# Performance work log

Hardware: AMD Instinct MI355X
Metric: run time of the kernel (lower is better)

The kernel has to match this reference:

```python
import jax, jax.numpy as jnp
from jax import lax
import numpy as np

IMG = 1024          # original image H = W
HD = WD = 256       # detection feature map (stride 4)
CD = 128            # detection feature channels
HS = WS = 512       # segmentation feature map (stride 2)
CS = 32             # segmentation feature channels
FC = 1024           # detection head conv / fc filters
K = 2000            # pre-NMS topk
MAX_OUT = 500       # max proposals after NMS
NMS_THR = 1.0       # distance threshold in detection-grid units
CROP = 48           # instance crop size (instance_crop_size // 2)
CI = 64             # instance conv channels


def _conv(x, w, b):
    # x: [H,W,Cin] single map -> same-padded conv
    y = lax.conv_general_dilated(x[None], w, (1, 1), 'SAME',
                                 dimension_numbers=('NHWC', 'HWIO', 'NHWC'))[0]
    return y + b


def _conv_b(x, w, b):
    # x: [N,H,W,Cin] batched conv
    y = lax.conv_general_dilated(x, w, (1, 1), 'SAME',
                                 dimension_numbers=('NHWC', 'HWIO', 'NHWC'))
    return y + b


def setup_inputs() -> dict:
    key = jax.random.key(0)
    ks = jax.random.split(key, 10)
    s = 0.02
    return {
        'detection_features': jax.random.normal(ks[0], (HD, WD, CD), jnp.float32),
        'segmentation_features': jax.random.normal(ks[1], (HS, WS, CS), jnp.float32),
        'Wc': jax.random.normal(ks[2], (3, 3, CD, FC), jnp.float32) * s,
        'bc': jnp.zeros((FC,), jnp.float32),
        'Wfc': jax.random.normal(ks[3], (1, 1, FC, FC), jnp.float32) * s,
        'bfc': jnp.zeros((FC,), jnp.float32),
        'Ws': jax.random.normal(ks[4], (1, 1, FC, 1), jnp.float32) * s,
        'bs': jnp.zeros((1,), jnp.float32),
        'Wr': jax.random.normal(ks[5], (1, 1, FC, 2), jnp.float32) * s,
        'br': jnp.zeros((2,), jnp.float32),
        'Wi': jax.random.normal(ks[6], (3, 3, CS, CI), jnp.float32) * s,
        'bi': jnp.zeros((CI,), jnp.float32),
        'Wo': jax.random.normal(ks[7], (3, 3, CI, 1), jnp.float32) * s,
        'bo': jnp.zeros((1,), jnp.float32),
    }


def _forward(detection_features, segmentation_features,
             Wc, bc, Wfc, bfc, Ws, bs, Wr, br, Wi, bi, Wo, bo):
    x = jax.nn.relu(_conv(detection_features, Wc, bc))
    x = jax.nn.relu(_conv(x, Wfc, bfc))
    scores = jax.nn.sigmoid(_conv(x, Ws, bs))[..., 0]          # [HD,WD]
    reg = _conv(x, Wr, br)                                      # [HD,WD,2] offsets in grid units

    # ---- proposal_locations: decode, topk, distance-threshold NMS ----
    yy, xx = jnp.meshgrid(jnp.arange(HD, dtype=jnp.float32),
                          jnp.arange(WD, dtype=jnp.float32), indexing='ij')
    ctr = jnp.stack([yy, xx], axis=-1) + 0.5                    # cell centers
    locs = (ctr + reg) / jnp.array([HD, WD], jnp.float32)       # normalized [0,1]
    flat_scores = scores.reshape(-1)                            # [HD*WD]
    flat_locs = locs.reshape(-1, 2)

    top_s, top_i = lax.top_k(flat_scores, K)                    # pre-NMS topk (sorted desc)
    cand = flat_locs[top_i]                                     # [K,2] normalized

    grid_xy = cand * jnp.array([HD, WD], jnp.float32)           # grid-unit coords
    d2 = jnp.sum((grid_xy[:, None, :] - grid_xy[None, :, :]) ** 2, axis=-1)  # [K,K]
    close = d2 < (NMS_THR * NMS_THR)
    later = jnp.arange(K)[None, :] > jnp.arange(K)[:, None]

    def nms_body(i, suppressed):
        keep_i = jnp.logical_not(suppressed[i])
        return suppressed | (keep_i & close[i] & later[i])

    suppressed = lax.fori_loop(0, K, nms_body, jnp.zeros((K,), jnp.bool_))
    masked = jnp.where(suppressed, -1.0, top_s)
    proposed_scores, sel = lax.top_k(masked, MAX_OUT)           # [500]
    sel_norm = cand[sel]                                        # [500,2]
    decoded = sel_norm * jnp.float32(IMG)                       # pixel coords

    # ---- instance head: crop stride-2 seg features around each proposal ----
    seg_loc = decoded / 2.0
    start = jnp.clip(jnp.round(seg_loc - CROP / 2), 0, HS - CROP).astype(jnp.int32)  # [500,2]

    def crop_one(st):
        return lax.dynamic_slice(segmentation_features, (st[0], st[1], 0), (CROP, CROP, CS))

    crops = jax.vmap(crop_one)(start)                           # [500,48,48,CS]
    h = jax.nn.relu(_conv_b(crops, Wi, bi))                     # [500,48,48,CI]
    instance_output = jax.nn.sigmoid(_conv_b(h, Wo, bo))        # [500,48,48,1]

    cy, cx = jnp.meshgrid(jnp.arange(CROP), jnp.arange(CROP), indexing='ij')
    instance_coords = start[:, None, None, :] + jnp.stack([cy, cx], axis=-1)[None]  # [500,48,48,2]

    return proposed_scores, decoded, instance_output, instance_coords


def reference(detection_features, segmentation_features,
              Wc, bc, Wfc, bfc, Ws, bs, Wr, br, Wi, bi, Wo, bo):
    return _forward(detection_features, segmentation_features,
                    Wc, bc, Wfc, bfc, Ws, bs, Wr, br, Wi, bi, Wo, bo)
```

## Files before the change

### kernel.cpp

```cpp
#include <hip/hip_runtime.h>
#include <math.h>

#define KTOP 2000
#define MAXOUT 500
#define CANDCAP 4096
#define NSEL 3600
#define RCC 32
#define RC2 16

typedef __attribute__((ext_vector_type(8))) short short8;
typedef __attribute__((ext_vector_type(4))) float f32x4;
typedef __attribute__((ext_vector_type(4))) double f64x4;

__device__ __forceinline__ unsigned short f2bf(float f) {
  unsigned int u = __float_as_uint(f);
  unsigned int r = ((u >> 16) & 1u) + 0x7FFFu;
  return (unsigned short)((u + r) >> 16);
}

__device__ __forceinline__ void ld_lds16(const void* g, void* l) {
  __builtin_amdgcn_global_load_lds((const unsigned int*)g, (unsigned int*)l,
                                   16, 0, 0);
}

__device__ __forceinline__ void hard_barrier() {
  asm volatile("" ::: "memory");
  __builtin_amdgcn_sched_barrier(0);
  __builtin_amdgcn_s_barrier();
  __builtin_amdgcn_sched_barrier(0);
  asm volatile("" ::: "memory");
}

__global__ __launch_bounds__(256) void transpose_bf16_kernel(
    const float* __restrict__ W, unsigned short* __restrict__ WT, int K, int N)
{
  __shared__ float t[32][33];
  const int k0 = blockIdx.x << 5, n0 = blockIdx.y << 5;
  const int tid = threadIdx.x;
  const int r = tid >> 5, c = tid & 31;
#pragma unroll
  for (int p = 0; p < 4; ++p)
    t[r + (p << 3)][c] = W[(size_t)(k0 + r + (p << 3)) * N + n0 + c];
  __syncthreads();
#pragma unroll
  for (int p = 0; p < 4; ++p)
    WT[(size_t)(n0 + r + (p << 3)) * K + k0 + c] = f2bf(t[c][r + (p << 3)]);
}

__global__ __launch_bounds__(256) void prep_wib_kernel(
    const float* __restrict__ Wi, unsigned short* __restrict__ WiB)
{
  const int t = blockIdx.x * 256 + threadIdx.x;
  if (t < 9 * 64 * 32) {
    const int tap = t / 2048, r = t & 2047, co = r >> 5, ci = r & 31;
    WiB[t] = f2bf(Wi[((size_t)tap * 32 + ci) * 64 + co]);
  }
}

__global__ __launch_bounds__(256) void pad_df_bf16(
    const float* __restrict__ df, unsigned short* __restrict__ dfb)
{
  const int t = blockIdx.x * 256 + threadIdx.x;
  if (t >= 258 * 258 * 16) return;
  const int p = t >> 4;
  const int c8 = (t & 15) << 3;
  const int gy = p / 258 - 1, gx = p % 258 - 1;
  uint4 out = make_uint4(0, 0, 0, 0);
  if (gy >= 0 && gy < 256 && gx >= 0 && gx < 256) {
    const float* src = &df[((size_t)(gy * 256 + gx)) * 128 + c8];
    const float4 v0 = *(const float4*)src;
    const float4 v1 = *(const float4*)(src + 4);
    out.x = (unsigned int)f2bf(v0.x) | ((unsigned int)f2bf(v0.y) << 16);
    out.y = (unsigned int)f2bf(v0.z) | ((unsigned int)f2bf(v0.w) << 16);
    out.z = (unsigned int)f2bf(v1.x) | ((unsigned int)f2bf(v1.y) << 16);
    out.w = (unsigned int)f2bf(v1.z) | ((unsigned int)f2bf(v1.w) << 16);
  }
  *(uint4*)&dfb[(size_t)p * 128 + c8] = out;
}

__device__ __forceinline__ void ktile_phases(
    const unsigned short* __restrict__ A0, const unsigned short* __restrict__ B0,
    const int arow, const int brow, const int ok0, const int ok1,
    f32x4 (&acc)[8][4])
{
  short8 Af[4][2], Bf[2][2][2];
#pragma unroll
  for (int m = 0; m < 4; ++m) {
    Af[m][0] = *(const short8*)&A0[((arow + (m << 4)) << 6) + ok0];
    Af[m][1] = *(const short8*)&A0[((arow + (m << 4)) << 6) + ok1];
  }
#pragma unroll
  for (int n = 0; n < 2; ++n) {
    Bf[0][n][0] = *(const short8*)&B0[((brow + (n << 4)) << 6) + ok0];
    Bf[0][n][1] = *(const short8*)&B0[((brow + (n << 4)) << 6) + ok1];
  }
  hard_barrier();
  __builtin_amdgcn_s_setprio(1);
#pragma unroll
  for (int m = 0; m < 4; ++m)
#pragma unroll
    for (int n = 0; n < 2; ++n) {
      acc[m][n] = __builtin_amdgcn_mfma_f32_16x16x32_bf16(Af[m][0], Bf[0][n][0], acc[m][n], 0, 0, 0);
      acc[m][n] = __builtin_amdgcn_mfma_f32_16x16x32_bf16(Af[m][1], Bf[0][n][1], acc[m][n], 0, 0, 0);
    }
  __builtin_amdgcn_s_setprio(0);
  hard_barrier();
#pragma unroll
  for (int n = 0; n < 2; ++n) {
    Bf[1][n][0] = *(const short8*)&B0[((brow + ((n + 2) << 4)) << 6) + ok0];
    Bf[1][n][1] = *(const short8*)&B0[((brow + ((n + 2) << 4)) << 6) + ok1];
  }
  hard_barrier();
  __builtin_amdgcn_s_setprio(1);
#pragma unroll
  for (int m = 0; m < 4; ++m)
#pragma unroll
    for (int n = 0; n < 2; ++n) {
      acc[m][n + 2] = __builtin_amdgcn_mfma_f32_16x16x32_bf16(Af[m][0], Bf[1][n][0], acc[m][n + 2], 0, 0, 0);
      acc[m][n + 2] = __builtin_amdgcn_mfma_f32_16x16x32_bf16(Af[m][1], Bf[1][n][1], acc[m][n + 2], 0, 0, 0);
    }
  __builtin_amdgcn_s_setprio(0);
  hard_barrier();
#pragma unroll
  for (int m = 0; m < 4; ++m) {
    Af[m][0] = *(const short8*)&A0[((arow + 64 + (m << 4)) << 6) + ok0];
    Af[m][1] = *(const short8*)&A0[((arow + 64 + (m << 4)) << 6) + ok1];
  }
  hard_barrier();
  __builtin_amdgcn_s_setprio(1);
#pragma unroll
  for (int m = 0; m < 4; ++m)
#pragma unroll
    for (int n = 0; n < 2; ++n) {
      acc[m + 4][n + 2] = __builtin_amdgcn_mfma_f32_16x16x32_bf16(Af[m][0], Bf[1][n][0], acc[m + 4][n + 2], 0, 0, 0);
      acc[m + 4][n + 2] = __builtin_amdgcn_mfma_f32_16x16x32_bf16(Af[m][1], Bf[1][n][1], acc[m + 4][n + 2], 0, 0, 0);
    }
  __builtin_amdgcn_s_setprio(0);
  hard_barrier();
  __builtin_amdgcn_s_setprio(1);
#pragma unroll
  for (int m = 0; m < 4; ++m)
#pragma unroll
    for (int n = 0; n < 2; ++n) {
      acc[m + 4][n] = __builtin_amdgcn_mfma_f32_16x16x32_bf16(Af[m][0], Bf[0][n][0], acc[m + 4][n], 0, 0, 0);
      acc[m + 4][n] = __builtin_amdgcn_mfma_f32_16x16x32_bf16(Af[m][1], Bf[0][n][1], acc[m + 4][n], 0, 0, 0);
    }
  __builtin_amdgcn_s_setprio(0);
  hard_barrier();
}

__global__ __launch_bounds__(512) void conv1_mfma(
    const unsigned short* __restrict__ dfb, const unsigned short* __restrict__ WcT,
    const float* __restrict__ bc, unsigned short* __restrict__ x1b, int pt0)
{
  __shared__ __align__(16) unsigned short smem[65536];
  const int tid = threadIdx.x;
  const int wv = tid >> 6, lane = tid & 63;
  const int wr = wv >> 2, wc = wv & 3;
  const int l15 = lane & 15, quad = lane >> 4;
  const int n0 = blockIdx.x << 8;
  const int lm0 = blockIdx.y << 8;
  const int Pbase = (pt0 << 6) + lm0;
  const int y = Pbase >> 8;
  const int tr = tid >> 3, g8 = tid & 7;
  const int xg = ((g8 ^ (tr & 7)) << 4);
  const int axr = l15 & 7;
  const int ok0 = ((quad ^ axr) << 3);
  const int ok1 = (((4 + quad) ^ axr) << 3);
  const int arow = (wr << 7) + l15;
  const int brow = (wc << 6) + l15;

  float bcv[4];
#pragma unroll
  for (int j = 0; j < 4; ++j) bcv[j] = bc[n0 + (wc << 6) + (j << 4) + l15];

  f32x4 acc[8][4];
  const f32x4 z4 = {0.f, 0.f, 0.f, 0.f};
#pragma unroll
  for (int i = 0; i < 8; ++i)
#pragma unroll
    for (int j = 0; j < 4; ++j) acc[i][j] = z4;

  const char* WB = (const char*)WcT + ((size_t)(n0 + tr) * 1152) * 2 + xg;
  unsigned short* lA = &smem[(tr << 6) + (g8 << 3)];

  auto issue = [&](int kt, int buf) {
    const int tap = kt >> 1, ci0 = (kt & 1) << 6;
    const int dy = tap / 3 - 1, dx = tap % 3 - 1;
    const char* Ab = (const char*)dfb +
        (((size_t)((y + dy + 1) * 258 + dx + 1)) * 128 + ci0) * 2 +
        (size_t)tr * 256 + xg;
    unsigned short* la = lA + buf * 32768;
    unsigned short* lb = la + 16384;
    const char* Bb = WB + (size_t)kt * 128;
#pragma unroll
    for (int i = 0; i < 4; ++i)
      ld_lds16(Ab + (size_t)i * 16384, la + i * 4096);
#pragma unroll
    for (int i = 0; i < 4; ++i)
      ld_lds16(Bb + (size_t)i * 147456, lb + i * 4096);
  };

  issue(0, 0);
  issue(1, 1);
#pragma unroll 2
  for (int kt = 0; kt < 18; ++kt) {
    const int buf = kt & 1;
    if (kt < 17) asm volatile("s_waitcnt vmcnt(8)" ::: "memory");
    else         asm volatile("s_waitcnt vmcnt(0)" ::: "memory");
    hard_barrier();
    ktile_phases(&smem[buf * 32768], &smem[buf * 32768 + 16384],
                 arow, brow, ok0, ok1, acc);
    if (kt < 16) issue(kt + 2, buf);
  }

#pragma unroll
  for (int m = 0; m < 8; ++m)
#pragma unroll
    for (int n = 0; n < 4; ++n) {
      const int col = n0 + (wc << 6) + (n << 4) + l15;
      const float bb = bcv[n];
#pragma unroll
      for (int rg = 0; rg < 4; ++rg) {
        const int row = lm0 + (wr << 7) + (m << 4) + (quad << 2) + rg;
        const float v = fmaxf(acc[m][n][rg] + bb, 0.f);
        x1b[(size_t)row * 1024 + col] = f2bf(v);
      }
    }
}

__global__ __launch_bounds__(512) void fc_mfma(
    const unsigned short* __restrict__ x1b, const unsigned short* __restrict__ WfcT,
    const float* __restrict__ bfc, const float* __restrict__ Wsc,
    float* __restrict__ part, int pt0)
{
  __shared__ __align__(16) unsigned short smem[65536];
  const int tid = threadIdx.x;
  const int wv = tid >> 6, lane = tid & 63;
  const int wr = wv >> 2, wc = wv & 3;
  const int l15 = lane & 15, quad = lane >> 4;
  const int n0 = blockIdx.x << 8;
  const int lm0 = blockIdx.y << 8;
  const int Pbase = (pt0 << 6) + lm0;
  const int tr = tid >> 3, g8 = tid & 7;
  const int xg = ((g8 ^ (tr & 7)) << 4);
  const int axr = l15 & 7;
  const int ok0 = ((quad ^ axr) << 3);
  const int ok1 = (((4 + quad) ^ axr) << 3);
  const int arow = (wr << 7) + l15;
  const int brow = (wc << 6) + l15;

  float wsv[4], bfv[4];
#pragma unroll
  for (int j = 0; j < 4; ++j) {
    const int col = n0 + (wc << 6) + (j << 4) + l15;
    wsv[j] = Wsc[col];
    bfv[j] = bfc[col];
  }

  f32x4 acc[8][4];
  const f32x4 z4 = {0.f, 0.f, 0.f, 0.f};
#pragma unroll
  for (int i = 0; i < 8; ++i)
#pragma unroll
    for (int j = 0; j < 4; ++j) acc[i][j] = z4;

  const char* AB = (const char*)x1b + ((size_t)(lm0 + tr) * 1024) * 2 + xg;
  const char* WB = (const char*)WfcT + ((size_t)(n0 + tr) * 1024) * 2 + xg;
  unsigned short* lA = &smem[(tr << 6) + (g8 << 3)];

  auto issue = [&](int kt, int buf) {
    unsigned short* la = lA + buf * 32768;
    unsigned short* lb = la + 16384;
    const char* Ab = AB + (size_t)kt * 128;
    const char* Bb = WB + (size_t)kt * 128;
#pragma unroll
    for (int i = 0; i < 4; ++i)
      ld_lds16(Ab + (size_t)i * 131072, la + i * 4096);
#pragma unroll
    for (int i = 0; i < 4; ++i)
      ld_lds16(Bb + (size_t)i * 131072, lb + i * 4096);
  };

  issue(0, 0);
  issue(1, 1);
#pragma unroll 2
  for (int kt = 0; kt < 16; ++kt) {
    const int buf = kt & 1;
    if (kt < 15) asm volatile("s_waitcnt vmcnt(8)" ::: "memory");
    else         asm volatile("s_waitcnt vmcnt(0)" ::: "memory");
    hard_barrier();
    ktile_phases(&smem[buf * 32768], &smem[buf * 32768 + 16384],
                 arow, brow, ok0, ok1, acc);
    if (kt < 14) issue(kt + 2, buf);
  }

  float* red = (float*)smem;
#pragma unroll
  for (int m = 0; m < 8; ++m)
#pragma unroll
    for (int rg = 0; rg < 4; ++rg) {
      float ps = 0.f;
#pragma unroll
      for (int n = 0; n < 4; ++n) {
        const float v = fmaxf(acc[m][n][rg] + bfv[n], 0.f);
        ps = fmaf(v, wsv[n], ps);
      }
#pragma unroll
      for (int off = 1; off <= 8; off <<= 1)
        ps += __shfl_xor(ps, off, 64);
      if (l15 == 0) {
        const int row = (wr << 7) + (m << 4) + (quad << 2) + rg;
        red[row * 5 + wc] = ps;
      }
    }
  __syncthreads();
  if (tid < 256) {
    float s = 0.f;
#pragma unroll
    for (int w8 = 0; w8 < 4; ++w8) s += red[tid * 5 + w8];
    part[(size_t)blockIdx.x * 65536 + Pbase + tid] = s;
  }
}

__global__ __launch_bounds__(256) void head_finalize_kernel(
    const float* __restrict__ part, const float* __restrict__ bs,
    float* __restrict__ scores)
{
  const int pix = blockIdx.x * 256 + threadIdx.x;
  float s = 0.f;
#pragma unroll
  for (int cb = 0; cb < 4; ++cb) s += part[(size_t)cb * 65536 + pix];
  s += bs[0];
  scores[pix] = 1.f / (1.f + expf(-s));
}

__global__ __launch_bounds__(1024) void select_kernel(
    const float* __restrict__ scores, unsigned int* __restrict__ cand_idx,
    unsigned int* __restrict__ cand_cnt)
{
  __shared__ unsigned int hist[256];
  __shared__ unsigned int sh_prefix, sh_sub;
  __shared__ int scan_s[1024];
  const int tid = threadIdx.x;

  unsigned int prefix = 0u;
  int need = NSEL;
  for (int byte = 3; byte >= 0; --byte) {
    if (tid < 256) hist[tid] = 0u;
    __syncthreads();
    const int sh = byte * 8;
    const unsigned int mhi = (byte == 3) ? 0u : (0xFFFFFFFFu << (sh + 8));
    for (int i = tid; i < 65536; i += 1024) {
      const unsigned int b = __float_as_uint(scores[i]);
      if ((b & mhi) == prefix) atomicAdd(&hist[(b >> sh) & 255u], 1u);
    }
    __syncthreads();
    for (int off = 1; off < 256; off <<= 1) {
      unsigned int add = 0u;
      if (tid < 256 && tid + off < 256) add = hist[tid + off];
      __syncthreads();
      if (tid < 256) hist[tid] += add;
      __syncthreads();
    }
    if (tid < 256) {
      const unsigned int sv = hist[tid];
      const unsigned int above = (tid == 255) ? 0u : hist[tid + 1];
      if ((int)above < need && (int)sv >= need) {
        sh_prefix = prefix | ((unsigned)tid << sh);
        sh_sub = above;
      }
    }
    __syncthreads();
    prefix = sh_prefix;
    need -= (int)sh_sub;
    __syncthreads();
  }
  const float thr = __uint_as_float(prefix);

  const int b0 = tid << 6;
  int my = 0;
  for (int k = 0; k < 64; ++k)
    if (scores[b0 + k] >= thr) ++my;
  scan_s[tid] = my;
  __syncthreads();
  for (int off = 1; off < 1024; off <<= 1) {
    const int a = scan_s[tid];
    const int b = (tid >= off) ? scan_s[tid - off] : 0;
    __syncthreads();
    scan_s[tid] = a + b;
    __syncthreads();
  }
  int pos = scan_s[tid] - my;
  const int total = scan_s[1023];
  for (int k = 0; k < 64; ++k) {
    if (scores[b0 + k] >= thr) {
      if (pos < CANDCAP) cand_idx[pos] = (unsigned int)(b0 + k);
      ++pos;
    }
  }
  if (tid == 0)
    *cand_cnt = (unsigned int)(total > CANDCAP ? CANDCAP : total);
}

#define PSTR 133
__global__ __launch_bounds__(512) void rescore_conv(
    const float* __restrict__ df, const float* __restrict__ Wc,
    const float* __restrict__ bc,
    const unsigned int* __restrict__ cand_idx,
    const unsigned int* __restrict__ cand_cnt,
    double* __restrict__ x1g)
{
  __shared__ double patt[RCC * PSTR];
  __shared__ int rrs[RCC], ccs[RCC];
  const int cnt = (int)*cand_cnt;
  const int nb = blockIdx.x & 1;
  const int c0 = (blockIdx.x >> 1) * RCC;
  if (c0 >= cnt) return;
  const int tid = threadIdx.x;
  const int wv = tid >> 6, lane = tid & 63;
  const int m = lane & 15, quad = lane >> 4;
  const int co_base = (nb << 9) + (wv << 6);

  if (tid < RCC) {
    const int slot = (c0 + tid < cnt) ? c0 + tid : c0;
    const unsigned int idx = cand_idx[slot];
    rrs[tid] = (int)(idx >> 8); ccs[tid] = (int)(idx & 255u);
  }

  f64x4 acc[2][4];
  const f64x4 z4 = {0.0, 0.0, 0.0, 0.0};
#pragma unroll
  for (int ct = 0; ct < 2; ++ct)
#pragma unroll
    for (int t = 0; t < 4; ++t) acc[ct][t] = z4;

  for (int tap = 0; tap < 9; ++tap) {
    const int dy = tap / 3 - 1, dx = tap % 3 - 1;
    __syncthreads();
    for (int p = tid; p < RCC * 128; p += 512) {
      const int c = p >> 7, ci = p & 127;
      const int gy = rrs[c] + dy, gx = ccs[c] + dx;
      float v = 0.f;
      if (gy >= 0 && gy < 256 && gx >= 0 && gx < 256)
        v = df[((size_t)((gy << 8) + gx)) * 128 + ci];
      patt[c * PSTR + ci] = (double)v;
    }
    __syncthreads();
    const float* wrow = &Wc[(size_t)(tap * 128 + quad) * 1024 + co_base + m];
    float wf[4];
#pragma unroll
    for (int t = 0; t < 4; ++t) wf[t] = wrow[t << 4];
    for (int k4 = 0; k4 < 32; ++k4) {
      float wn[4];
      if (k4 + 1 < 32) {
#pragma unroll
        for (int t = 0; t < 4; ++t)
          wn[t] = wrow[(size_t)((k4 + 1) << 2) * 1024 + (t << 4)];
      }
      const double a0 = patt[m * PSTR + (k4 << 2) + quad];
      const double a1 = patt[(16 + m) * PSTR + (k4 << 2) + quad];
#pragma unroll
      for (int t = 0; t < 4; ++t)
        acc[0][t] = __builtin_amdgcn_mfma_f64_16x16x4f64(a0, (double)wf[t], acc[0][t], 0, 0, 0);
#pragma unroll
      for (int t = 0; t < 4; ++t)
        acc[1][t] = __builtin_amdgcn_mfma_f64_16x16x4f64(a1, (double)wf[t], acc[1][t], 0, 0, 0);
      if (k4 + 1 < 32) {
#pragma unroll
        for (int t = 0; t < 4; ++t) wf[t] = wn[t];
      }
    }
  }
#pragma unroll
  for (int ct = 0; ct < 2; ++ct)
#pragma unroll
    for (int t = 0; t < 4; ++t) {
      const int co = co_base + (t << 4) + m;
      const double bb = (double)bc[co];
#pragma unroll
      for (int rg = 0; rg < 4; ++rg) {
        const int cand = (ct << 4) + (quad << 2) + rg;
        if (c0 + cand < cnt) {
          const double v = acc[ct][t][rg] + bb;
          x1g[(size_t)(c0 + cand) * 1024 + co] = v > 0.0 ? v : 0.0;
        }
      }
    }
}

__global__ __launch_bounds__(512) void rescore_fc(
    const double* __restrict__ x1g, const float* __restrict__ Wfc,
    const float* __restrict__ bfc, const float* __restrict__ Wsc,
    const float* __restrict__ bs, const float* __restrict__ Wrg,
    const float* __restrict__ br,
    const unsigned int* __restrict__ cand_cnt,
    unsigned long long* __restrict__ cand_sb,
    double* __restrict__ cand_ry, double* __restrict__ cand_rx)
{
  __shared__ double xbuf[16 * PSTR];
  __shared__ double partw[3][8][16];
  const int cnt = (int)*cand_cnt;
  const int c0 = blockIdx.x * RC2;
  if (c0 >= cnt) return;
  const int tid = threadIdx.x;
  const int wv = tid >> 6, lane = tid & 63;
  const int m = lane & 15, quad = lane >> 4;
  const int co_base = wv << 7;

  f64x4 acc[8];
  const f64x4 z4 = {0.0, 0.0, 0.0, 0.0};
#pragma unroll
  for (int t = 0; t < 8; ++t) acc[t] = z4;

  for (int kc = 0; kc < 8; ++kc) {
    __syncthreads();
    for (int p = tid; p < 2048; p += 512) {
      const int c = p >> 7, k = p & 127;
      const int row = (c0 + c < cnt) ? c0 + c : c0;
      xbuf[c * PSTR + k] = x1g[(size_t)row * 1024 + (kc << 7) + k];
    }
    __syncthreads();
    const float* wrow = &Wfc[(size_t)((kc << 7) + quad) * 1024 + co_base + m];
    float wf[8];
#pragma unroll
    for (int t = 0; t < 8; ++t) wf[t] = wrow[t << 4];
    for (int k4 = 0; k4 < 32; ++k4) {
      float wn[8];
      if (k4 + 1 < 32) {
#pragma unroll
        for (int t = 0; t < 8; ++t)
          wn[t] = wrow[(size_t)((k4 + 1) << 2) * 1024 + (t << 4)];
      }
      const double a = xbuf[m * PSTR + (k4 << 2) + quad];
#pragma unroll
      for (int t = 0; t < 8; ++t)
        acc[t] = __builtin_amdgcn_mfma_f64_16x16x4f64(a, (double)wf[t], acc[t], 0, 0, 0);
      if (k4 + 1 < 32) {
#pragma unroll
        for (int t = 0; t < 8; ++t) wf[t] = wn[t];
      }
    }
  }

  double ps[4] = {0, 0, 0, 0}, py[4] = {0, 0, 0, 0}, px[4] = {0, 0, 0, 0};
#pragma unroll
  for (int t = 0; t < 8; ++t) {
    const int co = co_base + (t << 4) + m;
    const double bfv = (double)bfc[co];
    const double wsv = (double)Wsc[co];
    const double w0 = (double)Wrg[co * 2], w1 = (double)Wrg[co * 2 + 1];
#pragma unroll
    for (int rg = 0; rg < 4; ++rg) {
      double v = acc[t][rg] + bfv;
      v = v > 0.0 ? v : 0.0;
      ps[rg] = fma(v, wsv, ps[rg]);
      py[rg] = fma(v, w0, py[rg]);
      px[rg] = fma(v, w1, px[rg]);
    }
  }
#pragma unroll
  for (int off = 1; off <= 8; off <<= 1) {
#pragma unroll
    for (int rg = 0; rg < 4; ++rg) {
      ps[rg] += __shfl_xor(ps[rg], off, 64);
      py[rg] += __shfl_xor(py[rg], off, 64);
      px[rg] += __shfl_xor(px[rg], off, 64);
    }
  }
  if (m == 0) {
#pragma unroll
    for (int rg = 0; rg < 4; ++rg) {
      const int cand = (quad << 2) + rg;
      partw[0][wv][cand] = ps[rg];
      partw[1][wv][cand] = py[rg];
      partw[2][wv][cand] = px[rg];
    }
  }
  __syncthreads();
  if (tid < 48) {
    const int cand = tid & 15, h = tid >> 4;
    double s = 0.0;
#pragma unroll
    for (int w8 = 0; w8 < 8; ++w8) s += partw[h][w8][cand];
    if (c0 + cand < cnt) {
      if (h == 0) {
        const double lg = s + (double)bs[0];
        const double sg = 1.0 / (1.0 + exp(-lg));
        cand_sb[c0 + cand] = (unsigned long long)__double_as_longlong(sg);
      } else if (h == 1) cand_ry[c0 + cand] = s + (double)br[0];
      else               cand_rx[c0 + cand] = s + (double)br[1];
    }
  }
}

#define PROP_LDS 102400
__global__ __launch_bounds__(1024) void proposal_kernel(
    const unsigned int* __restrict__ cand_idx,
    const unsigned int* __restrict__ cand_cnt,
    const unsigned long long* __restrict__ cand_sb,
    const double* __restrict__ cand_ry, const double* __restrict__ cand_rx,
    unsigned int* __restrict__ cellrank,
    double* __restrict__ cyg, double* __restrict__ cxg,
    int* __restrict__ startb, float* __restrict__ out_ps,
    float* __restrict__ out_dec)
{
  extern __shared__ __align__(16) char dynsm[];
  unsigned long long* sk = (unsigned long long*)dynsm;
  unsigned int* si = (unsigned int*)(dynsm + 16384);
  int* scan = (int*)(dynsm + 24576);
  unsigned short* nbrs = (unsigned short*)(dynsm + 32768);
  unsigned char* kept = (unsigned char*)(dynsm + 98304);
  unsigned char* nbrc = (unsigned char*)(dynsm + 100352);

  __shared__ unsigned int hist[256];
  __shared__ unsigned long long sh_pref;
  __shared__ unsigned int sh_sub;
  __shared__ volatile unsigned int changed;
  __shared__ int sh_maxreg;

  const int tid = threadIdx.x;
  const int cnt = (int)*cand_cnt;

  for (int i = tid; i < 65536; i += 1024) cellrank[i] = 0xFFFFFFFFu;

  unsigned long long prefix = 0ull;
  int need = KTOP;
  for (int byte = 7; byte >= 0; --byte) {
    if (tid < 256) hist[tid] = 0u;
    __syncthreads();
    const int sh = byte * 8;
    const unsigned long long mhi =
        (byte == 7) ? 0ull : (0xFFFFFFFFFFFFFFFFull << (sh + 8));
    for (int i = tid; i < cnt; i += 1024) {
      const unsigned long long k = cand_sb[i];
      if ((k & mhi) == prefix) atomicAdd(&hist[(unsigned int)((k >> sh) & 255u)], 1u);
    }
    __syncthreads();
    for (int off = 1; off < 256; off <<= 1) {
      unsigned int add = 0u;
      if (tid < 256 && tid + off < 256) add = hist[tid + off];
      __syncthreads();
      if (tid < 256) hist[tid] += add;
      __syncthreads();
    }
    if (tid < 256) {
      const unsigned int sv = hist[tid];
      const unsigned int above = (tid == 255) ? 0u : hist[tid + 1];
      if ((int)above < need && (int)sv >= need) {
        sh_pref = prefix | ((unsigned long long)(unsigned)tid << sh);
        sh_sub = above;
      }
    }
    __syncthreads();
    prefix = sh_pref;
    need -= (int)sh_sub;
    __syncthreads();
  }
  const unsigned long long T = prefix;

  const int s0 = tid << 2;
  unsigned long long kv[4];
  int ca = 0, cb = 0;
#pragma unroll
  for (int q = 0; q < 4; ++q) {
    const int s = s0 + q;
    kv[q] = (s < cnt) ? cand_sb[s] : 0ull;
    if (s < cnt) { if (kv[q] > T) ++ca; else if (kv[q] == T) ++cb; }
  }
  scan[tid] = ca;
  __syncthreads();
  for (int off = 1; off < 1024; off <<= 1) {
    const int a = scan[tid];
    const int b = (tid >= off) ? scan[tid - off] : 0;
    __syncthreads();
    scan[tid] = a + b;
    __syncthreads();
  }
  int posA = scan[tid] - ca;
  const int atot = scan[1023];
  __syncthreads();
  scan[tid] = cb;
  __syncthreads();
  for (int off = 1; off < 1024; off <<= 1) {
    const int a = scan[tid];
    const int b = (tid >= off) ? scan[tid - off] : 0;
    __syncthreads();
    scan[tid] = a + b;
    __syncthreads();
  }
  int posB = atot + (scan[tid] - cb);
  __syncthreads();
#pragma unroll
  for (int q = 0; q < 4; ++q) {
    const int s = s0 + q;
    if (s < cnt) {
      if (kv[q] > T) {
        sk[posA] = kv[q]; si[posA] = (unsigned int)s; ++posA;
      } else if (kv[q] == T) {
        if (posB < KTOP) { sk[posB] = kv[q]; si[posB] = (unsigned int)s; }
        ++posB;
      }
    }
  }
  __syncthreads();
  for (int i = tid; i < 2048; i += 1024)
    if (i >= KTOP) { sk[i] = 0ull; si[i] = 0u; }
  if (tid == 0) sh_maxreg = 0;
  __syncthreads();

  for (int k = 2; k <= 2048; k <<= 1) {
    for (int j = k >> 1; j > 0; j >>= 1) {
      const int i = (tid & (j - 1)) | ((tid & ~(j - 1)) << 1);
      const int ixj = i | j;
      const unsigned long long a = sk[i], b = sk[ixj];
      const unsigned int ia = si[i], ib = si[ixj];
      const bool up = ((i & k) == 0);
      const bool lt = (a < b) || (a == b && ia > ib);
      const bool gt = (a > b) || (a == b && ia < ib);
      if (up ? lt : gt) {
        sk[i] = b; sk[ixj] = a;
        si[i] = ib; si[ixj] = ia;
      }
      __syncthreads();
    }
  }

  for (int r = tid; r < KTOP; r += 1024) {
    const unsigned int slot = si[r];
    const unsigned int idx = cand_idx[slot];
    const int row = (int)(idx >> 8), col = (int)(idx & 255u);
    const double ry = cand_ry[slot], rx = cand_rx[slot];
    cyg[r] = ((double)row + 0.5) + ry;
    cxg[r] = ((double)col + 0.5) + rx;
    kept[r] = 1; nbrc[r] = 0;
    cellrank[idx] = (unsigned int)r;
    atomicMax(&sh_maxreg, __float_as_int((float)fabs(ry)));
    atomicMax(&sh_maxreg, __float_as_int((float)fabs(rx)));
  }
  __syncthreads();
  const float maxreg = __int_as_float(sh_maxreg);
  int rad = (int)(1.0f + 2.0f * maxreg) + 1;
  if (rad > 8) rad = 8;
  if (rad < 1) rad = 1;

  for (int r = tid; r < KTOP; r += 1024) {
    const unsigned int idx = cand_idx[si[r]];
    const int row = (int)(idx >> 8), col = (int)(idx & 255u);
    int n = 0;
    const double pyr = cyg[r], pxr = cxg[r];
    for (int dy = -rad; dy <= rad; ++dy) {
      const int yy = row + dy; if (yy < 0 || yy >= 256) continue;
      for (int dx = -rad; dx <= rad; ++dx) {
        if (dy == 0 && dx == 0) continue;
        const int xx = col + dx; if (xx < 0 || xx >= 256) continue;
        const unsigned int q = cellrank[yy * 256 + xx];
        if (q < (unsigned int)r) {
          const double t1 = __dsub_rn(pyr, cyg[q]);
          const double t2 = __dsub_rn(pxr, cxg[q]);
          const double d2 = __dadd_rn(__dmul_rn(t1, t1), __dmul_rn(t2, t2));
          if (d2 < 1.0) { if (n < 16) nbrs[(r << 4) + n] = (unsigned short)q; ++n; }
        }
      }
    }
    nbrc[r] = (unsigned char)(n < 16 ? n : 16);
  }
  __syncthreads();

  for (int it = 0; it < 4096; ++it) {
    __syncthreads();
    if (tid == 0) changed = 0;
    __syncthreads();
    for (int r = tid; r < KTOP; r += 1024) {
      const int nc = nbrc[r];
      if (nc) {
        int kvv = 1;
        for (int t = 0; t < nc; ++t)
          if (kept[nbrs[(r << 4) + t]]) { kvv = 0; break; }
        if (kvv != (int)kept[r]) { kept[r] = (unsigned char)kvv; changed = 1; }
      }
    }
    __syncthreads();
    if (changed == 0) break;
  }

  scan[tid]        = (tid < KTOP) ? (int)kept[tid] : 0;
  scan[tid + 1024] = (tid + 1024 < KTOP) ? (int)kept[tid + 1024] : 0;
  __syncthreads();
  for (int off = 1; off < 2048; off <<= 1) {
    const int a0 = scan[tid];
    const int b0 = (tid >= off) ? scan[tid - off] : 0;
    const int a1 = scan[tid + 1024];
    const int b1 = (tid + 1024 >= off) ? scan[tid + 1024 - off] : 0;
    __syncthreads();
    scan[tid] = a0 + b0;
    scan[tid + 1024] = a1 + b1;
    __syncthreads();
  }
  const int total = scan[KTOP - 1];

  for (int r = tid; r < KTOP; r += 1024) {
    int slot = -1;
    if (kept[r]) { const int p = scan[r] - 1; if (p < MAXOUT) slot = p; }
    else { const int p = total + (r - scan[r]); if (p < MAXOUT) slot = p; }
    if (slot >= 0) {
      const double sg = __longlong_as_double((long long)sk[r]);
      out_ps[slot] = kept[r] ? (float)sg : -1.0f;
      const double py = cyg[r], px = cxg[r];
      out_dec[slot * 2]     = (float)(py * 4.0);
      out_dec[slot * 2 + 1] = (float)(px * 4.0);
      int sy = (int)rint(py * 2.0 - 24.0);
      int sx = (int)rint(px * 2.0 - 24.0);
      sy = sy < 0 ? 0 : (sy > 464 ? 464 : sy);
      sx = sx < 0 ? 0 : (sx > 464 ? 464 : sx);
      startb[slot * 2] = sy; startb[slot * 2 + 1] = sx;
    }
  }
}

#define ISTR 40
__global__ __launch_bounds__(256) void conv_i_mfma(
    const float* __restrict__ seg, const unsigned short* __restrict__ WiB,
    const float* __restrict__ bi, const int* __restrict__ startb,
    unsigned short* __restrict__ h, int inst0)
{
  __shared__ __align__(16) unsigned short ins[500 * ISTR];
  const int li = blockIdx.y;
  const int inst = inst0 + li;
  const int tile = blockIdx.x;
  const int r0 = tile << 3;
  const int tid = threadIdx.x;
  const int sy = startb[inst * 2], sx = startb[inst * 2 + 1];

  for (int p = tid; p < 500; p += 256) {
    const int rr = p / 50, cc2 = p - rr * 50;
    const int ir = r0 - 1 + rr, ic = cc2 - 1;
    unsigned short* dst = &ins[p * ISTR];
    if (ir >= 0 && ir < 48 && ic >= 0 && ic < 48) {
      const float* src = &seg[((size_t)(sy + ir) * 512 + (sx + ic)) * 32];
#pragma unroll
      for (int q = 0; q < 8; ++q) {
        const float4 v = *(const float4*)&src[q << 2];
        const unsigned int lo = (unsigned int)f2bf(v.x) | ((unsigned int)f2bf(v.y) << 16);
        const unsigned int hi = (unsigned int)f2bf(v.z) | ((unsigned int)f2bf(v.w) << 16);
        *(uint2*)&dst[q << 2] = make_uint2(lo, hi);
      }
    } else {
#pragma unroll
      for (int q = 0; q < 4; ++q) *(uint4*)&dst[q << 3] = make_uint4(0, 0, 0, 0);
    }
  }
  __syncthreads();

  const int wv = tid >> 6, lane = tid & 63;
  const int l15 = lane & 15, quad = lane >> 4;
  const int wmb = wv * 96;

  int pbase[6];
#pragma unroll
  for (int i = 0; i < 6; ++i) {
    const int m = wmb + (i << 4) + l15;
    pbase[i] = (m / 48 + 1) * 50 + (m % 48) + 1;
  }

  f32x4 acc[6][4];
  const f32x4 z4 = {0.f, 0.f, 0.f, 0.f};
#pragma unroll
  for (int i = 0; i < 6; ++i)
#pragma unroll
    for (int j = 0; j < 4; ++j) acc[i][j] = z4;

  for (int tap = 0; tap < 9; ++tap) {
    const int off = (tap / 3 - 1) * 50 + (tap % 3 - 1);
    short8 b[4];
#pragma unroll
    for (int j = 0; j < 4; ++j)
      b[j] = *(const short8*)&WiB[((tap << 6) + (j << 4) + l15) * 32 + (quad << 3)];
#pragma unroll
    for (int i = 0; i < 6; ++i) {
      const short8 a = *(const short8*)&ins[(pbase[i] + off) * ISTR + (quad << 3)];
#pragma unroll
      for (int j = 0; j < 4; ++j)
        acc[i][j] = __builtin_amdgcn_mfma_f32_16x16x32_bf16(a, b[j], acc[i][j], 0, 0, 0);
    }
  }

  float bv[4];
#pragma unroll
  for (int j = 0; j < 4; ++j) bv[j] = bi[(j << 4) + l15];

  for (int half = 0; half < 2; ++half) {
    __syncthreads();
    if ((wv >> 1) == half) {
#pragma unroll
      for (int i = 0; i < 6; ++i)
#pragma unroll
        for (int j = 0; j < 4; ++j)
#pragma unroll
          for (int rg = 0; rg < 4; ++rg) {
            const int m = wmb + (i << 4) + (quad << 2) + rg;
            const int pp = m - half * 192;
            const float v = fmaxf(acc[i][j][rg] + bv[j], 0.f);
            ins[pp * 72 + (j << 4) + l15] = f2bf(v);
          }
    }
    __syncthreads();
    for (int t = tid; t < 192 * 8; t += 256) {
      const int pp = t >> 3, c8 = t & 7;
      const uint4 v = *(const uint4*)&ins[pp * 72 + (c8 << 3)];
      *(uint4*)&h[((size_t)li * 2304 + (tile * 384 + half * 192 + pp)) * 64 + (c8 << 3)] = v;
    }
  }
}

__global__ __launch_bounds__(256) void conv_o_kernel(
    const unsigned short* __restrict__ h, const float* __restrict__ Wo,
    const float* __restrict__ bo, const int* __restrict__ startb,
    float* __restrict__ out_io, float* __restrict__ out_ic, int inst0)
{
  __shared__ __align__(16) unsigned short hs[324 * 72];
  __shared__ float wos[576];
  const int li = blockIdx.y;
  const int inst = inst0 + li;
  const int tile = blockIdx.x;
  const int ty0 = (tile / 3) << 4;
  const int tx0 = (tile % 3) << 4;
  const int tid = threadIdx.x;

  for (int i = tid; i < 576; i += 256) wos[i] = Wo[i];
  for (int p = tid; p < 324; p += 256) {
    const int iy = p / 18, ix = p - iy * 18;
    const int gy = ty0 - 1 + iy, gx = tx0 - 1 + ix;
    unsigned short* dst = &hs[p * 72];
    if (gy >= 0 && gy < 48 && gx >= 0 && gx < 48) {
      const unsigned short* src = &h[((size_t)li * 2304 + gy * 48 + gx) * 64];
#pragma unroll
      for (int q = 0; q < 8; ++q) *(uint4*)&dst[q << 3] = *(const uint4*)&src[q << 3];
    } else {
#pragma unroll
      for (int q = 0; q < 8; ++q) *(uint4*)&dst[q << 3] = make_uint4(0, 0, 0, 0);
    }
  }
  __syncthreads();

  const int ly = tid >> 4, lx = tid & 15;
  float a = 0.f;
#pragma unroll
  for (int ky = 0; ky < 3; ++ky)
#pragma unroll
    for (int kx = 0; kx < 3; ++kx) {
      const unsigned short* hp = &hs[((ly + ky) * 18 + lx + kx) * 72];
      const float* wp = &wos[(ky * 3 + kx) << 6];
#pragma unroll
      for (int c8 = 0; c8 < 8; ++c8) {
        const uint4 hv = *(const uint4*)&hp[c8 << 3];
        const unsigned int uu[4] = {hv.x, hv.y, hv.z, hv.w};
#pragma unroll
        for (int e = 0; e < 4; ++e) {
          const float f0 = __uint_as_float(uu[e] << 16);
          const float f1 = __uint_as_float(uu[e] & 0xFFFF0000u);
          a = fmaf(f0, wp[(c8 << 3) + (e << 1)], a);
          a = fmaf(f1, wp[(c8 << 3) + (e << 1) + 1], a);
        }
      }
    }
  a += bo[0];
  const float o = 1.f / (1.f + expf(-a));
  const int gy = ty0 + ly, gx = tx0 + lx;
  const size_t p = ((size_t)inst * 48 + gy) * 48 + gx;
  out_io[p] = o;
  const int sy = startb[inst * 2], sx = startb[inst * 2 + 1];
  out_ic[p * 2]     = (float)(sy + gy);
  out_ic[p * 2 + 1] = (float)(sx + gx);
}

extern "C" void kernel_launch(void* const* d_in, const int* in_sizes, int n_in,
                              void* d_out, int out_size, void* d_ws, size_t ws_size,
                              hipStream_t stream)
{
  const float* df  = (const float*)d_in[0];
  const float* seg = (const float*)d_in[1];
  const float* Wc  = (const float*)d_in[2];
  const float* bc  = (const float*)d_in[3];
  const float* Wfc = (const float*)d_in[4];
  const float* bfc = (const float*)d_in[5];
  const float* Wsc = (const float*)d_in[6];
  const float* bs  = (const float*)d_in[7];
  const float* Wrg = (const float*)d_in[8];
  const float* br  = (const float*)d_in[9];
  const float* Wi  = (const float*)d_in[10];
  const float* bi  = (const float*)d_in[11];
  const float* Wo  = (const float*)d_in[12];
  const float* bo  = (const float*)d_in[13];

  const size_t SZ_WCT = 2359296ull, SZ_WFT = 2097152ull, SZ_WIB = 36864ull,
               SZ_DFB = 17040384ull,
               SZ_PART = 2097152ull, SZ_SC = 262144ull, SZ_CR = 262144ull,
               SZ_STB = 4096ull, SZ_CI = CANDCAP * 4ull,
               SZ_SB = CANDCAP * 8ull, SZ_RY = CANDCAP * 8ull,
               SZ_RX = CANDCAP * 8ull, SZ_CY = 16384ull, SZ_CX = 16384ull,
               SZ_X1G = (size_t)CANDCAP * 1024ull * 8ull,
               SZ_CNT = 256ull;
  const size_t FIXED = SZ_WCT + SZ_WFT + SZ_WIB + SZ_DFB + SZ_PART + SZ_SC +
                       SZ_CR + SZ_STB + SZ_CI + SZ_SB + SZ_RY + SZ_RX +
                       SZ_CY + SZ_CX + SZ_X1G + SZ_CNT;
  char* w = (char*)d_ws;
  size_t region = (ws_size > FIXED) ? ((ws_size - FIXED) & ~(size_t)255) : 0;
  char* fb = w + region;
  unsigned short* WcT = (unsigned short*)fb;   fb += SZ_WCT;
  unsigned short* WfcT = (unsigned short*)fb;  fb += SZ_WFT;
  unsigned short* WiB = (unsigned short*)fb;   fb += SZ_WIB;
  unsigned short* dfb = (unsigned short*)fb;   fb += SZ_DFB;
  float* part = (float*)fb;                    fb += SZ_PART;
  float* scores = (float*)fb;                  fb += SZ_SC;
  unsigned int* cellrank = (unsigned int*)fb;  fb += SZ_CR;
  int* startb = (int*)fb;                      fb += SZ_STB;
  unsigned int* cand_idx = (unsigned int*)fb;  fb += SZ_CI;
  unsigned long long* cand_sb = (unsigned long long*)fb; fb += SZ_SB;
  double* cand_ry = (double*)fb;               fb += SZ_RY;
  double* cand_rx = (double*)fb;               fb += SZ_RX;
  double* cyg = (double*)fb;                   fb += SZ_CY;
  double* cxg = (double*)fb;                   fb += SZ_CX;
  double* x1g = (double*)fb;                   fb += SZ_X1G;
  unsigned int* cand_cnt = (unsigned int*)fb;
  unsigned short* x1b = (unsigned short*)w;
  unsigned short* hb = (unsigned short*)w;

  size_t tiles_fit = region / 131072ull;
  int pt_chunk = 4;
  while ((size_t)(pt_chunk * 2) <= tiles_fit && pt_chunk < 1024) pt_chunk <<= 1;
  size_t inst_fit = region / 294912ull;
  const int opts[12] = {500, 250, 125, 100, 50, 25, 20, 10, 5, 4, 2, 1};
  int inst_chunk = 1;
  for (int o = 0; o < 12; ++o)
    if ((size_t)opts[o] <= inst_fit) { inst_chunk = opts[o]; break; }

  float* out = (float*)d_out;
  float* out_ps  = out;
  float* out_dec = out + 500;
  float* out_io  = out + 1500;
  float* out_ic  = out + 1153500;

  transpose_bf16_kernel<<<dim3(36, 32), 256, 0, stream>>>(Wc, WcT, 1152, 1024);
  transpose_bf16_kernel<<<dim3(32, 32), 256, 0, stream>>>(Wfc, WfcT, 1024, 1024);
  prep_wib_kernel<<<72, 256, 0, stream>>>(Wi, WiB);
  pad_df_bf16<<<4161, 256, 0, stream>>>(df, dfb);

  for (int c = 0; c < 1024 / pt_chunk; ++c) {
    conv1_mfma<<<dim3(4, pt_chunk / 4), 512, 0, stream>>>(dfb, WcT, bc, x1b,
                                                          c * pt_chunk);
    fc_mfma<<<dim3(4, pt_chunk / 4), 512, 0, stream>>>(x1b, WfcT, bfc, Wsc,
                                                       part, c * pt_chunk);
  }
  head_finalize_kernel<<<256, 256, 0, stream>>>(part, bs, scores);
  select_kernel<<<1, 1024, 0, stream>>>(scores, cand_idx, cand_cnt);
  rescore_conv<<<(CANDCAP / RCC) * 2, 512, 0, stream>>>(df, Wc, bc, cand_idx,
                                                        cand_cnt, x1g);
  rescore_fc<<<CANDCAP / RC2, 512, 0, stream>>>(x1g, Wfc, bfc, Wsc, bs, Wrg,
                                                br, cand_cnt, cand_sb,
                                                cand_ry, cand_rx);
  proposal_kernel<<<1, 1024, PROP_LDS, stream>>>(cand_idx, cand_cnt, cand_sb,
                                                 cand_ry, cand_rx, cellrank,
                                                 cyg, cxg, startb, out_ps,
                                                 out_dec);
  for (int c = 0; c < 500 / inst_chunk; ++c) {
    conv_i_mfma<<<dim3(6, inst_chunk), 256, 0, stream>>>(seg, WiB, bi, startb,
                                                         hb, c * inst_chunk);
    conv_o_kernel<<<dim3(9, inst_chunk), 256, 0, stream>>>(hb, Wo, bo, startb,
                                                           out_io, out_ic,
                                                           c * inst_chunk);
  }
}
```

Before: 1.147 ms.

## Double-buffer LDS staging and deepen weight prefetch in rescore conv and fc

Both rescore kernels now load the next tap's or next K-chunk's activation tile into registers while the MFMA loop runs on the current LDS buffer. The registers are written to a second LDS buffer afterwards, which leaves one barrier per iteration instead of two. The weight register prefetch is also deepened from one k4 step ahead to two. The goal is to hide global-load latency behind the FP64 MFMA work, at the cost of doubled LDS use and higher register pressure, which may reduce occupancy.

```diff
diff --git a/kernel.cpp b/kernel.cpp
--- a/kernel.cpp
+++ b/kernel.cpp
@@ -411,7 +411,7 @@
     const unsigned int* __restrict__ cand_cnt,
     double* __restrict__ x1g)
 {
-  __shared__ double patt[RCC * PSTR];
+  __shared__ double patt[2][RCC * PSTR];
   __shared__ int rrs[RCC], ccs[RCC];
   const int cnt = (int)*cand_cnt;
   const int nb = blockIdx.x & 1;
@@ -427,39 +427,59 @@
     const unsigned int idx = cand_idx[slot];
     rrs[tid] = (int)(idx >> 8); ccs[tid] = (int)(idx & 255u);
   }
-
-  f64x4 acc[2][4];
-  const f64x4 z4 = {0.0, 0.0, 0.0, 0.0};
-#pragma unroll
-  for (int ct = 0; ct < 2; ++ct)
-#pragma unroll
-    for (int t = 0; t < 4; ++t) acc[ct][t] = z4;
-
-  for (int tap = 0; tap < 9; ++tap) {
+  __syncthreads();
+
+  float sv[8];
+  auto ldregs = [&](int tap) {
     const int dy = tap / 3 - 1, dx = tap % 3 - 1;
-    __syncthreads();
-    for (int p = tid; p < RCC * 128; p += 512) {
+#pragma unroll
+    for (int j = 0; j < 8; ++j) {
+      const int p = tid + (j << 9);
       const int c = p >> 7, ci = p & 127;
       const int gy = rrs[c] + dy, gx = ccs[c] + dx;
       float v = 0.f;
       if (gy >= 0 && gy < 256 && gx >= 0 && gx < 256)
         v = df[((size_t)((gy << 8) + gx)) * 128 + ci];
-      patt[c * PSTR + ci] = (double)v;
-    }
-    __syncthreads();
+      sv[j] = v;
+    }
+  };
+  auto wrlds = [&](int b) {
+#pragma unroll
+    for (int j = 0; j < 8; ++j) {
+      const int p = tid + (j << 9);
+      const int c = p >> 7, ci = p & 127;
+      patt[b][c * PSTR + ci] = (double)sv[j];
+    }
+  };
+
+  f64x4 acc[2][4];
+  const f64x4 z4 = {0.0, 0.0, 0.0, 0.0};
+#pragma unroll
+  for (int ct = 0; ct < 2; ++ct)
+#pragma unroll
+    for (int t = 0; t < 4; ++t) acc[ct][t] = z4;
+
+  ldregs(0);
+  wrlds(0);
+  __syncthreads();
+  int buf = 0;
+  for (int tap = 0; tap < 9; ++tap) {
+    if (tap < 8) ldregs(tap + 1);
     const float* wrow = &Wc[(size_t)(tap * 128 + quad) * 1024 + co_base + m];
-    float wf[4];
+    float wf[4], wn[4];
 #pragma unroll
     for (int t = 0; t < 4; ++t) wf[t] = wrow[t << 4];
+#pragma unroll
+    for (int t = 0; t < 4; ++t) wn[t] = wrow[(size_t)4096 + (t << 4)];
     for (int k4 = 0; k4 < 32; ++k4) {
-      float wn[4];
-      if (k4 + 1 < 32) {
+      float w2[4];
+      if (k4 + 2 < 32) {
 #pragma unroll
         for (int t = 0; t < 4; ++t)
-          wn[t] = wrow[(size_t)((k4 + 1) << 2) * 1024 + (t << 4)];
-      }
-      const double a0 = patt[m * PSTR + (k4 << 2) + quad];
-      const double a1 = patt[(16 + m) * PSTR + (k4 << 2) + quad];
+          w2[t] = wrow[(size_t)((k4 + 2) << 2) * 1024 + (t << 4)];
+      }
+      const double a0 = patt[buf][m * PSTR + (k4 << 2) + quad];
+      const double a1 = patt[buf][(16 + m) * PSTR + (k4 << 2) + quad];
 #pragma unroll
       for (int t = 0; t < 4; ++t)
         acc[0][t] = __builtin_amdgcn_mfma_f64_16x16x4f64(a0, (double)wf[t], acc[0][t], 0, 0, 0);
@@ -470,7 +490,14 @@
 #pragma unroll
         for (int t = 0; t < 4; ++t) wf[t] = wn[t];
       }
-    }
+      if (k4 + 2 < 32) {
+#pragma unroll
+        for (int t = 0; t < 4; ++t) wn[t] = w2[t];
+      }
+    }
+    if (tap < 8) wrlds(buf ^ 1);
+    __syncthreads();
+    buf ^= 1;
   }
 #pragma unroll
   for (int ct = 0; ct < 2; ++ct)
@@ -498,7 +525,7 @@
     unsigned long long* __restrict__ cand_sb,
     double* __restrict__ cand_ry, double* __restrict__ cand_rx)
 {
-  __shared__ double xbuf[16 * PSTR];
+  __shared__ double xbuf[2][16 * PSTR];
   __shared__ double partw[3][8][16];
   const int cnt = (int)*cand_cnt;
   const int c0 = blockIdx.x * RC2;
@@ -508,31 +535,50 @@
   const int m = lane & 15, quad = lane >> 4;
   const int co_base = wv << 7;
 
+  double sx[4];
+  auto ldregs = [&](int kc) {
+#pragma unroll
+    for (int j = 0; j < 4; ++j) {
+      const int p = tid + (j << 9);
+      const int c = p >> 7, k = p & 127;
+      const int row = (c0 + c < cnt) ? c0 + c : c0;
+      sx[j] = x1g[(size_t)row * 1024 + (kc << 7) + k];
+    }
+  };
+  auto wrlds = [&](int b) {
+#pragma unroll
+    for (int j = 0; j < 4; ++j) {
+      const int p = tid + (j << 9);
+      const int c = p >> 7, k = p & 127;
+      xbuf[b][c * PSTR + k] = sx[j];
+    }
+  };
+
   f64x4 acc[8];
   const f64x4 z4 = {0.0, 0.0, 0.0, 0.0};
 #pragma unroll
   for (int t = 0; t < 8; ++t) acc[t] = z4;
 
+  ldregs(0);
+  wrlds(0);
+  __syncthreads();
+  int buf = 0;
   for (int kc = 0; kc < 8; ++kc) {
-    __syncthreads();
-    for (int p = tid; p < 2048; p += 512) {
-      const int c = p >> 7, k = p & 127;
-      const int row = (c0 + c < cnt) ? c0 + c : c0;
-      xbuf[c * PSTR + k] = x1g[(size_t)row * 1024 + (kc << 7) + k];
-    }
-    __syncthreads();
+    if (kc < 7) ldregs(kc + 1);
     const float* wrow = &Wfc[(size_t)((kc << 7) + quad) * 1024 + co_base + m];
-    float wf[8];
+    float wf[8], wn[8];
 #pragma unroll
     for (int t = 0; t < 8; ++t) wf[t] = wrow[t << 4];
+#pragma unroll
+    for (int t = 0; t < 8; ++t) wn[t] = wrow[(size_t)4096 + (t << 4)];
     for (int k4 = 0; k4 < 32; ++k4) {
-      float wn[8];
-      if (k4 + 1 < 32) {
+      float w2[8];
+      if (k4 + 2 < 32) {
 #pragma unroll
         for (int t = 0; t < 8; ++t)
-          wn[t] = wrow[(size_t)((k4 + 1) << 2) * 1024 + (t << 4)];
-      }
-      const double a = xbuf[m * PSTR + (k4 << 2) + quad];
+          w2[t] = wrow[(size_t)((k4 + 2) << 2) * 1024 + (t << 4)];
+      }
+      const double a = xbuf[buf][m * PSTR + (k4 << 2) + quad];
 #pragma unroll
       for (int t = 0; t < 8; ++t)
         acc[t] = __builtin_amdgcn_mfma_f64_16x16x4f64(a, (double)wf[t], acc[t], 0, 0, 0);
@@ -540,7 +586,14 @@
 #pragma unroll
         for (int t = 0; t < 8; ++t) wf[t] = wn[t];
       }
-    }
+      if (k4 + 2 < 32) {
+#pragma unroll
+        for (int t = 0; t < 8; ++t) wn[t] = w2[t];
+      }
+    }
+    if (kc < 7) wrlds(buf ^ 1);
+    __syncthreads();
+    buf ^= 1;
   }
 
   double ps[4] = {0, 0, 0, 0}, py[4] = {0, 0, 0, 0}, px[4] = {0, 0, 0, 0};
```

Result: no change. 1.169 ms (+1.9%).
